# Optimization experiments

Measured on AMD Instinct MI355X. Metric: run time of the kernel, lower is better.

Reference implementation:

```python
import jax, jax.numpy as jnp
import numpy as np

NUM_CLASSES = 50000
NUM_SAMPLED = 1000
D_MODEL = 1024
BATCH, SEQ = 32, 512


def _log_expected_count(ids, num_sampled, num_classes):
    # TF log-uniform candidate sampler (unique=True):
    # P(c) = log((c+2)/(c+1)) / log(num_classes+1)
    # E[count] = -expm1(num_sampled * log1p(-P))
    ids_f = ids.astype(jnp.float32)
    p = (jnp.log(ids_f + 2.0) - jnp.log(ids_f + 1.0)) / np.float32(np.log(num_classes + 1.0))
    return jnp.log(-jnp.expm1(num_sampled * jnp.log1p(-p)))


def setup_inputs() -> dict:
    key = jax.random.key(0)
    k1, k2, k3, k4 = jax.random.split(key, 4)
    lstm_outputs = jax.random.normal(k1, (BATCH, SEQ, D_MODEL), dtype=jnp.float32)
    next_token_ids = jax.random.randint(k2, (BATCH, SEQ), 0, NUM_CLASSES)
    sampled_ids = jax.random.randint(k3, (BATCH, NUM_SAMPLED), 0, NUM_CLASSES)
    W = jax.random.normal(k4, (NUM_CLASSES, D_MODEL), dtype=jnp.float32) * (1.0 / np.sqrt(D_MODEL))
    b = jnp.zeros((NUM_CLASSES,), dtype=jnp.float32)
    return {"lstm_outputs": lstm_outputs, "next_token_ids": next_token_ids,
            "sampled_ids": sampled_ids, "W": W, "b": b}


def reference(lstm_outputs, next_token_ids, sampled_ids, W, b):
    # Vectorized sampled-softmax loss (tf.nn.sampled_softmax_loss with
    # log-uniform sampler, partition_strategy irrelevant, accidental-hit removal),
    # mapped over the batch dim as the original tf.map_fn does.
    log_q_true = _log_expected_count(next_token_ids, NUM_SAMPLED, NUM_CLASSES)   # [B,T]
    log_q_samp = _log_expected_count(sampled_ids, NUM_SAMPLED, NUM_CLASSES)      # [B,S]

    w_true = W[next_token_ids]                                                   # [B,T,D]
    true_logit = (jnp.einsum('btd,btd->bt', lstm_outputs, w_true)
                  + b[next_token_ids] - log_q_true)                              # [B,T]

    w_samp = W[sampled_ids]                                                      # [B,S,D]
    samp_logits = (jnp.einsum('btd,bsd->bts', lstm_outputs, w_samp)
                   + b[sampled_ids][:, None, :] - log_q_samp[:, None, :])        # [B,T,S]

    # remove accidental hits (sampled id == true label)
    hit = sampled_ids[:, None, :] == next_token_ids[:, :, None]                  # [B,T,S]
    samp_logits = jnp.where(hit, jnp.float32(-1e9), samp_logits)

    all_logits = jnp.concatenate([true_logit[..., None], samp_logits], axis=-1)  # [B,T,1+S]
    # softmax CE with true class at index 0
    losses = jax.nn.logsumexp(all_logits, axis=-1) - true_logit                  # [B,T]
    return 0.5 * jnp.mean(losses)
```

## Files before the change

### kernel.cpp

```cpp
#include <hip/hip_runtime.h>
#include <cmath>

#define BATCH 32
#define SEQLEN 512
#define NSAMP 1000
#define DMODEL 1024
#define NCHUNK 4

typedef __bf16 bf16x8_t __attribute__((ext_vector_type(8)));
typedef float f32x4_t __attribute__((ext_vector_type(4)));

__device__ __forceinline__ unsigned pack_bf2(float lo, float hi) {
    unsigned ulo = __float_as_uint(lo);
    unsigned uhi = __float_as_uint(hi);
    ulo = (ulo + 0x7fffu + ((ulo >> 16) & 1u)) >> 16;
    uhi = (uhi + 0x7fffu + ((uhi >> 16) & 1u)) & 0xffff0000u;
    return (ulo & 0xffffu) | uhi;
}

__device__ __forceinline__ float log_expected_count(int id) {
    float idf = (float)id;
    float p = log1pf(1.0f / (idf + 1.0f)) * 0.09242316f;
    return logf(-expm1f(1000.0f * log1pf(-p)));
}

__device__ __forceinline__ void gl16(const void* g, void* l) {
    __builtin_amdgcn_global_load_lds(
        (const __attribute__((address_space(1))) unsigned int*)g,
        (__attribute__((address_space(3))) unsigned int*)l,
        16, 0, 0);
}

__global__ __launch_bounds__(256) void prep_kernel(
    const float* __restrict__ h, const int* __restrict__ labels,
    const int* __restrict__ sids, const float* __restrict__ W,
    const float* __restrict__ bias, unsigned short* __restrict__ Wb,
    unsigned short* __restrict__ hb,
    float* __restrict__ adjw, float* __restrict__ tlw)
{
    const int w = threadIdx.x >> 6, lane = threadIdx.x & 63;
    if (blockIdx.x < 8000) {
        const int row = blockIdx.x * 4 + w;
        const int sv = sids[row];
        const float4* src = (const float4*)(W + (size_t)sv * DMODEL);
        unsigned short* dst = Wb + (size_t)row * DMODEL;
#pragma unroll
        for (int j = 0; j < 4; ++j) {
            float4 v = src[lane + j * 64];
            uint2 u;
            u.x = pack_bf2(v.x, v.y);
            u.y = pack_bf2(v.z, v.w);
            *(uint2*)(dst + (lane + j * 64) * 4) = u;
        }
        if (lane == 0) adjw[row] = bias[sv] - log_expected_count(sv);
    } else {
        const int r = (blockIdx.x - 8000) * 4 + w;
        const int lab = labels[r];
        const float4* hp = (const float4*)(h + (size_t)r * DMODEL);
        const float4* wp = (const float4*)(W + (size_t)lab * DMODEL);
        unsigned short* hdst = hb + (size_t)r * DMODEL;
        float s = 0.0f;
#pragma unroll
        for (int j = 0; j < 4; ++j) {
            float4 a = hp[lane + j * 64];
            float4 c = wp[lane + j * 64];
            s += a.x * c.x + a.y * c.y + a.z * c.z + a.w * c.w;
            uint2 u;
            u.x = pack_bf2(a.x, a.y);
            u.y = pack_bf2(a.z, a.w);
            *(uint2*)(hdst + (lane + j * 64) * 4) = u;
        }
#pragma unroll
        for (int off = 32; off > 0; off >>= 1) s += __shfl_xor(s, off, 64);
        if (lane == 0) tlw[r] = s + bias[lab] - log_expected_count(lab);
    }
}

__global__ __launch_bounds__(512, 2) void sampled_softmax_main(
    const int* __restrict__ labels, const int* __restrict__ sids,
    const unsigned short* __restrict__ hb, const unsigned short* __restrict__ Wb,
    const float* __restrict__ adjw,
    float* __restrict__ pm, float* __restrict__ pl)
{
    __shared__ __align__(16) unsigned short Ab[2][256 * 64];
    __shared__ __align__(16) unsigned short Bb[2][256 * 64];
    __shared__ int   sid_lds[256];
    __shared__ float adj_lds[256];
    __shared__ int   lab_lds[256];
    __shared__ float mpart[4][256];
    __shared__ float lpart[4][256];

    const int wg     = blockIdx.x;
    const int bb     = wg & 31;
    const int rest   = wg >> 5;
    const int tile_t = rest & 1;
    const int chunk  = rest >> 1;
    const int t0  = tile_t * 256;
    const int tid = threadIdx.x;
    const int wv  = tid >> 6, l = tid & 63;
    const int wr  = wv >> 2, wc = wv & 3;
    const int lm  = l & 15,  q = l >> 4;
    const int rl8 = l >> 3,  cp8 = l & 7;

    if (tid < 256) {
        const int s = chunk * 256 + tid;
        const bool v = s < NSAMP;
        sid_lds[tid] = v ? sids[bb * NSAMP + s] : -1;
        adj_lds[tid] = v ? adjw[bb * NSAMP + s] : 0.0f;
        lab_lds[tid] = labels[bb * SEQLEN + t0 + tid];
    }

    const int csg = (cp8 ^ rl8) * 8;
    const unsigned short* aSrc = hb + (size_t)(bb * SEQLEN + t0 + 32 * wv + rl8) * DMODEL + csg;
    const unsigned short* bSrc[4];
#pragma unroll
    for (int j = 0; j < 4; ++j) {
        int rb = chunk * 256 + 32 * wv + 8 * j + rl8;
        if (rb > NSAMP - 1) rb = NSAMP - 1;
        bSrc[j] = Wb + (size_t)(bb * NSAMP + rb) * DMODEL + csg;
    }

#define STAGE_TILE(KT, BUF)                                                   \
    do {                                                                      \
        const size_t _adv = (size_t)(KT) * 64;                                \
        gl16(aSrc + _adv,                 &Ab[BUF][(32 * wv     ) * 64]);     \
        gl16(aSrc + 8 * DMODEL + _adv,    &Ab[BUF][(32 * wv +  8) * 64]);     \
        gl16(aSrc + 16 * DMODEL + _adv,   &Ab[BUF][(32 * wv + 16) * 64]);     \
        gl16(aSrc + 24 * DMODEL + _adv,   &Ab[BUF][(32 * wv + 24) * 64]);     \
        gl16(bSrc[0] + _adv, &Bb[BUF][(32 * wv     ) * 64]);                  \
        gl16(bSrc[1] + _adv, &Bb[BUF][(32 * wv +  8) * 64]);                  \
        gl16(bSrc[2] + _adv, &Bb[BUF][(32 * wv + 16) * 64]);                  \
        gl16(bSrc[3] + _adv, &Bb[BUF][(32 * wv + 24) * 64]);                  \
    } while (0)

    const int ck0 = ((0 + q) ^ (lm & 7)) * 8;
    const int ck1 = ((4 + q) ^ (lm & 7)) * 8;
    int rowA[8], rowB[4];
#pragma unroll
    for (int t = 0; t < 8; ++t) rowA[t] = (128 * wr + 16 * t + lm) * 64;
#pragma unroll
    for (int c = 0; c < 4; ++c) rowB[c] = (64 * wc + 16 * c + lm) * 64;

    f32x4_t acc[8][4];
#pragma unroll
    for (int t = 0; t < 8; ++t)
#pragma unroll
        for (int c = 0; c < 4; ++c) acc[t][c] = (f32x4_t){0.f, 0.f, 0.f, 0.f};

    STAGE_TILE(0, 0);
    STAGE_TILE(1, 1);
    asm volatile("s_waitcnt lgkmcnt(0)" ::: "memory");
    __builtin_amdgcn_s_barrier();

#pragma unroll
    for (int kt = 0; kt < 16; ++kt) {
        if (kt < 15) { asm volatile("s_waitcnt vmcnt(8)" ::: "memory"); }
        else         { asm volatile("s_waitcnt vmcnt(0)" ::: "memory"); }
        __builtin_amdgcn_s_barrier();

        const unsigned short* Ac = Ab[kt & 1];
        const unsigned short* Bc = Bb[kt & 1];
#pragma unroll
        for (int s = 0; s < 2; ++s) {
            const int ck = s ? ck1 : ck0;
            bf16x8_t fa[8];
#pragma unroll
            for (int t = 0; t < 8; ++t) fa[t] = *(const bf16x8_t*)(Ac + rowA[t] + ck);
            __builtin_amdgcn_s_setprio(1);
#pragma unroll
            for (int c = 0; c < 4; ++c) {
                bf16x8_t fb = *(const bf16x8_t*)(Bc + rowB[c] + ck);
#pragma unroll
                for (int t = 0; t < 8; ++t)
                    acc[t][c] = __builtin_amdgcn_mfma_f32_16x16x32_bf16(fa[t], fb, acc[t][c], 0, 0, 0);
            }
            __builtin_amdgcn_s_setprio(0);
        }

        if (kt + 2 < 16) {
            __builtin_amdgcn_s_barrier();
            STAGE_TILE(kt + 2, kt & 1);
        }
    }
#undef STAGE_TILE

    float adjv[4]; int sidv[4]; bool cval[4];
#pragma unroll
    for (int c = 0; c < 4; ++c) {
        const int col = 64 * wc + 16 * c + lm;
        adjv[c] = adj_lds[col];
        sidv[c] = sid_lds[col];
        cval[c] = (chunk * 256 + col) < NSAMP;
    }
#pragma unroll
    for (int t = 0; t < 8; ++t) {
#pragma unroll
        for (int i = 0; i < 4; ++i) {
            const int r = 128 * wr + 16 * t + 4 * q + i;
            const int lab = lab_lds[r];
            float x[4]; bool ok[4];
            float m = -INFINITY;
#pragma unroll
            for (int c = 0; c < 4; ++c) {
                x[c] = acc[t][c][i] + adjv[c];
                ok[c] = cval[c] && (sidv[c] != lab);
                if (ok[c]) m = fmaxf(m, x[c]);
            }
            float ls = 0.0f;
#pragma unroll
            for (int c = 0; c < 4; ++c) ls += ok[c] ? __expf(x[c] - m) : 0.0f;
#pragma unroll
            for (int off = 1; off < 16; off <<= 1) {
                const float mo = __shfl_xor(m, off, 64);
                const float lo = __shfl_xor(ls, off, 64);
                const float M  = fmaxf(m, mo);
                const float e1 = (ls > 0.0f) ? ls * __expf(m - M) : 0.0f;
                const float e2 = (lo > 0.0f) ? lo * __expf(mo - M) : 0.0f;
                m = M; ls = e1 + e2;
            }
            if (lm == 0) { mpart[wc][r] = m; lpart[wc][r] = ls; }
        }
    }
    __syncthreads();
    if (tid < 256) {
        float m = -INFINITY, lsum = 0.0f;
#pragma unroll
        for (int p = 0; p < 4; ++p) {
            const float mp = mpart[p][tid];
            const float lp = lpart[p][tid];
            if (lp > 0.0f) {
                if (mp > m) { lsum = lsum * __expf(m - mp) + lp; m = mp; }
                else        { lsum += lp * __expf(mp - m); }
            }
        }
        const int idx = (bb * SEQLEN + t0 + tid) * NCHUNK + chunk;
        pm[idx] = m;
        pl[idx] = lsum;
    }
}

__global__ __launch_bounds__(256) void combine_kernel(
    const float* __restrict__ pm, const float* __restrict__ pl,
    const float* __restrict__ tlw, float* __restrict__ bsum)
{
    __shared__ float wsum[4];
    const int tid = threadIdx.x;
    const int w = tid >> 6, lane = tid & 63;
    const int idx = blockIdx.x * 256 + tid;
    float m = -INFINITY, l = 0.0f;
#pragma unroll
    for (int c = 0; c < NCHUNK; ++c) {
        const float mp = pm[idx * NCHUNK + c];
        const float lp = pl[idx * NCHUNK + c];
        if (lp > 0.0f) {
            if (mp > m) { l = l * __expf(m - mp) + lp; m = mp; }
            else        { l += lp * __expf(mp - m); }
        }
    }
    const float t = tlw[idx];
    const float M = fmaxf(m, t);
    float loss = __logf(l * __expf(m - M) + __expf(t - M)) + M - t;
#pragma unroll
    for (int off = 32; off > 0; off >>= 1) loss += __shfl_xor(loss, off, 64);
    if (lane == 0) wsum[w] = loss;
    __syncthreads();
    if (tid == 0) bsum[blockIdx.x] = wsum[0] + wsum[1] + wsum[2] + wsum[3];
}

__global__ void finalize_kernel(const float* __restrict__ bsum, float* __restrict__ out) {
    float v = bsum[threadIdx.x];
#pragma unroll
    for (int off = 32; off > 0; off >>= 1) v += __shfl_xor(v, off, 64);
    if (threadIdx.x == 0) out[0] = v * (0.5f / (float)(BATCH * SEQLEN));
}

extern "C" void kernel_launch(void* const* d_in, const int* in_sizes, int n_in,
                              void* d_out, int out_size, void* d_ws, size_t ws_size,
                              hipStream_t stream) {
    const float* h      = (const float*)d_in[0];
    const int*   labels = (const int*)d_in[1];
    const int*   sids   = (const int*)d_in[2];
    const float* W      = (const float*)d_in[3];
    const float* bias   = (const float*)d_in[4];

    char* base = (char*)d_ws;
    unsigned short* Wb = (unsigned short*)base;
    unsigned short* hb = (unsigned short*)(base + 65536000);
    float* adjw = (float*)(base + 99090432);
    float* tlw  = (float*)(base + 99218432);
    float* pmw  = (float*)(base + 99283968);
    float* plw  = (float*)(base + 99546112);
    float* bsum = (float*)(base + 99808256);

    prep_kernel<<<dim3(12096), dim3(256), 0, stream>>>(h, labels, sids, W, bias, Wb, hb, adjw, tlw);
    sampled_softmax_main<<<dim3(256), dim3(512), 0, stream>>>(
        labels, sids, hb, Wb, adjw, pmw, plw);
    combine_kernel<<<dim3(64), dim3(256), 0, stream>>>(pmw, plw, tlw, bsum);
    finalize_kernel<<<dim3(1), dim3(64), 0, stream>>>(bsum, (float*)d_out);
}
```

Baseline: 384.9 us.

## Fuse sampled-weight gather and bf16 conversion into main GEMM kernel

The prep kernel no longer gathers the sampled W rows into a bf16 workspace. The main kernel now loads fp32 W rows directly through registers, packs them to bf16 and writes them to LDS, and it computes the bias/log-q adjustment inline. This removes the 64 MB workspace write and its read-back, at the cost of a single LDS buffer per stage. The pipeline changes from two tiles in flight to one tile of prefetch, and each main block reads fp32 W twice (both t-tiles), so global traffic in the main kernel rises.

Measured after the change: 375.2 us. -2.5%, faster.

```diff
diff --git a/kernel.cpp b/kernel.cpp
--- a/kernel.cpp
+++ b/kernel.cpp
@@ -33,53 +33,35 @@
 
 __global__ __launch_bounds__(256) void prep_kernel(
     const float* __restrict__ h, const int* __restrict__ labels,
-    const int* __restrict__ sids, const float* __restrict__ W,
-    const float* __restrict__ bias, unsigned short* __restrict__ Wb,
-    unsigned short* __restrict__ hb,
-    float* __restrict__ adjw, float* __restrict__ tlw)
+    const float* __restrict__ W, const float* __restrict__ bias,
+    unsigned short* __restrict__ hb, float* __restrict__ tlw)
 {
     const int w = threadIdx.x >> 6, lane = threadIdx.x & 63;
-    if (blockIdx.x < 8000) {
-        const int row = blockIdx.x * 4 + w;
-        const int sv = sids[row];
-        const float4* src = (const float4*)(W + (size_t)sv * DMODEL);
-        unsigned short* dst = Wb + (size_t)row * DMODEL;
-#pragma unroll
-        for (int j = 0; j < 4; ++j) {
-            float4 v = src[lane + j * 64];
-            uint2 u;
-            u.x = pack_bf2(v.x, v.y);
-            u.y = pack_bf2(v.z, v.w);
-            *(uint2*)(dst + (lane + j * 64) * 4) = u;
-        }
-        if (lane == 0) adjw[row] = bias[sv] - log_expected_count(sv);
-    } else {
-        const int r = (blockIdx.x - 8000) * 4 + w;
-        const int lab = labels[r];
-        const float4* hp = (const float4*)(h + (size_t)r * DMODEL);
-        const float4* wp = (const float4*)(W + (size_t)lab * DMODEL);
-        unsigned short* hdst = hb + (size_t)r * DMODEL;
-        float s = 0.0f;
-#pragma unroll
-        for (int j = 0; j < 4; ++j) {
-            float4 a = hp[lane + j * 64];
-            float4 c = wp[lane + j * 64];
-            s += a.x * c.x + a.y * c.y + a.z * c.z + a.w * c.w;
-            uint2 u;
-            u.x = pack_bf2(a.x, a.y);
-            u.y = pack_bf2(a.z, a.w);
-            *(uint2*)(hdst + (lane + j * 64) * 4) = u;
-        }
-#pragma unroll
-        for (int off = 32; off > 0; off >>= 1) s += __shfl_xor(s, off, 64);
-        if (lane == 0) tlw[r] = s + bias[lab] - log_expected_count(lab);
-    }
+    const int r = blockIdx.x * 4 + w;
+    const int lab = labels[r];
+    const float4* hp = (const float4*)(h + (size_t)r * DMODEL);
+    const float4* wp = (const float4*)(W + (size_t)lab * DMODEL);
+    unsigned short* hdst = hb + (size_t)r * DMODEL;
+    float s = 0.0f;
+#pragma unroll
+    for (int j = 0; j < 4; ++j) {
+        float4 a = hp[lane + j * 64];
+        float4 c = wp[lane + j * 64];
+        s += a.x * c.x + a.y * c.y + a.z * c.z + a.w * c.w;
+        uint2 u;
+        u.x = pack_bf2(a.x, a.y);
+        u.y = pack_bf2(a.z, a.w);
+        *(uint2*)(hdst + (lane + j * 64) * 4) = u;
+    }
+#pragma unroll
+    for (int off = 32; off > 0; off >>= 1) s += __shfl_xor(s, off, 64);
+    if (lane == 0) tlw[r] = s + bias[lab] - log_expected_count(lab);
 }
 
 __global__ __launch_bounds__(512, 2) void sampled_softmax_main(
     const int* __restrict__ labels, const int* __restrict__ sids,
-    const unsigned short* __restrict__ hb, const unsigned short* __restrict__ Wb,
-    const float* __restrict__ adjw,
+    const unsigned short* __restrict__ hb, const float* __restrict__ W,
+    const float* __restrict__ bias,
     float* __restrict__ pm, float* __restrict__ pl)
 {
     __shared__ __align__(16) unsigned short Ab[2][256 * 64];
@@ -104,33 +86,64 @@
 
     if (tid < 256) {
         const int s = chunk * 256 + tid;
-        const bool v = s < NSAMP;
-        sid_lds[tid] = v ? sids[bb * NSAMP + s] : -1;
-        adj_lds[tid] = v ? adjw[bb * NSAMP + s] : 0.0f;
+        if (s < NSAMP) {
+            const int sv = sids[bb * NSAMP + s];
+            sid_lds[tid] = sv;
+            adj_lds[tid] = bias[sv] - log_expected_count(sv);
+        } else {
+            sid_lds[tid] = -1;
+            adj_lds[tid] = 0.0f;
+        }
         lab_lds[tid] = labels[bb * SEQLEN + t0 + tid];
     }
 
     const int csg = (cp8 ^ rl8) * 8;
     const unsigned short* aSrc = hb + (size_t)(bb * SEQLEN + t0 + 32 * wv + rl8) * DMODEL + csg;
-    const unsigned short* bSrc[4];
+
+    const float* wsrc[4];
+    int bwoff[4];
 #pragma unroll
     for (int j = 0; j < 4; ++j) {
         int rb = chunk * 256 + 32 * wv + 8 * j + rl8;
         if (rb > NSAMP - 1) rb = NSAMP - 1;
-        bSrc[j] = Wb + (size_t)(bb * NSAMP + rb) * DMODEL + csg;
-    }
-
-#define STAGE_TILE(KT, BUF)                                                   \
+        const int sv = sids[bb * NSAMP + rb];
+        wsrc[j] = W + (size_t)sv * DMODEL + cp8 * 8;
+        bwoff[j] = (32 * wv + 8 * j + rl8) * 64 + (cp8 ^ rl8) * 8;
+    }
+
+    float4 br[8];
+#define LOAD_B(KT)                                                            \
+    do {                                                                      \
+        br[0] = *(const float4*)(wsrc[0] + (KT) * 64);                        \
+        br[1] = *(const float4*)(wsrc[0] + (KT) * 64 + 4);                    \
+        br[2] = *(const float4*)(wsrc[1] + (KT) * 64);                        \
+        br[3] = *(const float4*)(wsrc[1] + (KT) * 64 + 4);                    \
+        br[4] = *(const float4*)(wsrc[2] + (KT) * 64);                        \
+        br[5] = *(const float4*)(wsrc[2] + (KT) * 64 + 4);                    \
+        br[6] = *(const float4*)(wsrc[3] + (KT) * 64);                        \
+        br[7] = *(const float4*)(wsrc[3] + (KT) * 64 + 4);                    \
+    } while (0)
+
+#define PACK_WRITE_B(BUF)                                                     \
+    do {                                                                      \
+        _Pragma("unroll")                                                     \
+        for (int j = 0; j < 4; ++j) {                                         \
+            uint4 u;                                                          \
+            u.x = pack_bf2(br[2 * j].x, br[2 * j].y);                         \
+            u.y = pack_bf2(br[2 * j].z, br[2 * j].w);                         \
+            u.z = pack_bf2(br[2 * j + 1].x, br[2 * j + 1].y);                 \
+            u.w = pack_bf2(br[2 * j + 1].z, br[2 * j + 1].w);                 \
+            *(uint4*)&Bb[BUF][bwoff[j]] = u;                                  \
+        }                                                                     \
+    } while (0)
+
+#define STAGE_A(KT, BUF)                                                      \
     do {                                                                      \
         const size_t _adv = (size_t)(KT) * 64;                                \
-        gl16(aSrc + _adv,                 &Ab[BUF][(32 * wv     ) * 64]);     \
-        gl16(aSrc + 8 * DMODEL + _adv,    &Ab[BUF][(32 * wv +  8) * 64]);     \
-        gl16(aSrc + 16 * DMODEL + _adv,   &Ab[BUF][(32 * wv + 16) * 64]);     \
-        gl16(aSrc + 24 * DMODEL + _adv,   &Ab[BUF][(32 * wv + 24) * 64]);     \
-        gl16(bSrc[0] + _adv, &Bb[BUF][(32 * wv     ) * 64]);                  \
-        gl16(bSrc[1] + _adv, &Bb[BUF][(32 * wv +  8) * 64]);                  \
-        gl16(bSrc[2] + _adv, &Bb[BUF][(32 * wv + 16) * 64]);                  \
-        gl16(bSrc[3] + _adv, &Bb[BUF][(32 * wv + 24) * 64]);                  \
+        gl16(aSrc + _adv,               &Ab[BUF][(32 * wv     ) * 64]);       \
+        gl16(aSrc + 8 * DMODEL + _adv,  &Ab[BUF][(32 * wv +  8) * 64]);       \
+        gl16(aSrc + 16 * DMODEL + _adv, &Ab[BUF][(32 * wv + 16) * 64]);       \
+        gl16(aSrc + 24 * DMODEL + _adv, &Ab[BUF][(32 * wv + 24) * 64]);       \
     } while (0)
 
     const int ck0 = ((0 + q) ^ (lm & 7)) * 8;
@@ -147,19 +160,28 @@
 #pragma unroll
         for (int c = 0; c < 4; ++c) acc[t][c] = (f32x4_t){0.f, 0.f, 0.f, 0.f};
 
-    STAGE_TILE(0, 0);
-    STAGE_TILE(1, 1);
+    LOAD_B(0);
+    __builtin_amdgcn_sched_barrier(0);
+    STAGE_A(0, 0);
+    asm volatile("s_waitcnt vmcnt(0)" ::: "memory");
+    PACK_WRITE_B(0);
     asm volatile("s_waitcnt lgkmcnt(0)" ::: "memory");
     __builtin_amdgcn_s_barrier();
 
 #pragma unroll
     for (int kt = 0; kt < 16; ++kt) {
-        if (kt < 15) { asm volatile("s_waitcnt vmcnt(8)" ::: "memory"); }
-        else         { asm volatile("s_waitcnt vmcnt(0)" ::: "memory"); }
-        __builtin_amdgcn_s_barrier();
-
-        const unsigned short* Ac = Ab[kt & 1];
-        const unsigned short* Bc = Bb[kt & 1];
+        const int cur = kt & 1, nxt = cur ^ 1;
+        if (kt + 1 < 16) {
+            LOAD_B(kt + 1);
+            __builtin_amdgcn_sched_barrier(0);
+            STAGE_A(kt + 1, nxt);
+            asm volatile("s_waitcnt vmcnt(12)" ::: "memory");
+        } else {
+            asm volatile("s_waitcnt vmcnt(0)" ::: "memory");
+        }
+
+        const unsigned short* Ac = Ab[cur];
+        const unsigned short* Bc = Bb[cur];
 #pragma unroll
         for (int s = 0; s < 2; ++s) {
             const int ck = s ? ck1 : ck0;
@@ -177,12 +199,16 @@
             __builtin_amdgcn_s_setprio(0);
         }
 
-        if (kt + 2 < 16) {
+        if (kt + 1 < 16) {
+            asm volatile("s_waitcnt vmcnt(4)" ::: "memory");
+            PACK_WRITE_B(nxt);
+            asm volatile("s_waitcnt lgkmcnt(0)" ::: "memory");
             __builtin_amdgcn_s_barrier();
-            STAGE_TILE(kt + 2, kt & 1);
-        }
-    }
-#undef STAGE_TILE
+        }
+    }
+#undef LOAD_B
+#undef PACK_WRITE_B
+#undef STAGE_A
 
     float adjv[4]; int sidv[4]; bool cval[4];
 #pragma unroll
@@ -284,17 +310,15 @@
     const float* bias   = (const float*)d_in[4];
 
     char* base = (char*)d_ws;
-    unsigned short* Wb = (unsigned short*)base;
-    unsigned short* hb = (unsigned short*)(base + 65536000);
-    float* adjw = (float*)(base + 99090432);
-    float* tlw  = (float*)(base + 99218432);
-    float* pmw  = (float*)(base + 99283968);
-    float* plw  = (float*)(base + 99546112);
-    float* bsum = (float*)(base + 99808256);
-
-    prep_kernel<<<dim3(12096), dim3(256), 0, stream>>>(h, labels, sids, W, bias, Wb, hb, adjw, tlw);
+    unsigned short* hb = (unsigned short*)base;
+    float* tlw  = (float*)(base + 33554432);
+    float* pmw  = (float*)(base + 33619968);
+    float* plw  = (float*)(base + 33882112);
+    float* bsum = (float*)(base + 34144256);
+
+    prep_kernel<<<dim3(4096), dim3(256), 0, stream>>>(h, labels, W, bias, hb, tlw);
     sampled_softmax_main<<<dim3(256), dim3(512), 0, stream>>>(
-        labels, sids, hb, Wb, adjw, pmw, plw);
+        labels, sids, hb, W, bias, pmw, plw);
     combine_kernel<<<dim3(64), dim3(256), 0, stream>>>(pmw, plw, tlw, bsum);
     finalize_kernel<<<dim3(1), dim3(64), 0, stream>>>(bsum, (float*)d_out);
 }
```
